# Optimization experiments

Measured on AMD Instinct MI355X. Metric: run time of the kernel, lower is better.

The kernel has to match this reference:

```python
import math
import jax, jax.numpy as jnp
import numpy as np

B, N, G, D = 8, 1000, 1000, 2
E, H = 128, 8           # embedding_dim, n_heads
DH = E // H             # head dim
KNN = 16                # n_decoding_neighbors (static: mask all zeros -> K=min(16,N))
TANH_CLIP = 10.0


def make_heads(x, n_heads):
    # (B, n, E) -> (B, n_heads, n, E//n_heads)
    b, n, e = x.shape
    return x.reshape(b, n, n_heads, e // n_heads).transpose(0, 2, 1, 3)


def setup_inputs() -> dict:
    key = jax.random.key(0)
    ks = jax.random.split(key, 12)
    s = 1.0 / math.sqrt(E)
    return {
        "last_node": jax.random.randint(ks[0], (B, G), 0, N),
        "coordinates": jax.random.uniform(ks[1], (B, N, D), dtype=jnp.float32),
        "embeddings": jax.random.normal(ks[2], (B, N, E), dtype=jnp.float32),
        "group_ninf_mask": jnp.zeros((B, G, N), dtype=jnp.float32),
        "Wq_graph": jax.random.normal(ks[3], (E, E), dtype=jnp.float32) * s,
        "Wq_first": jax.random.normal(ks[4], (E, E), dtype=jnp.float32) * s,
        "Wq_last": jax.random.normal(ks[5], (E, E), dtype=jnp.float32) * s,
        "Wk": jax.random.normal(ks[6], (E, E), dtype=jnp.float32) * s,
        "Wv": jax.random.normal(ks[7], (E, E), dtype=jnp.float32) * s,
        "W_comb": jax.random.normal(ks[8], (E, E), dtype=jnp.float32) * s,
        "b_comb": jax.random.normal(ks[9], (E,), dtype=jnp.float32) * s,
    }


def reference(last_node, coordinates, embeddings, group_ninf_mask,
              Wq_graph, Wq_first, Wq_last, Wk, Wv, W_comb, b_comb):
    # --- reset() precomputation ---
    graph_emb = embeddings.mean(axis=1, keepdims=True)          # (B,1,E)
    q_graph = make_heads(graph_emb @ Wq_graph.T, H)             # (B,H,1,DH)
    k_h = make_heads(embeddings @ Wk.T, H)                      # (B,H,N,DH)
    v_h = make_heads(embeddings @ Wv.T, H)                      # (B,H,N,DH)

    # --- gather last node embedding ---
    idx_e = jnp.broadcast_to(last_node[..., None], (B, G, E))
    last_emb = jnp.take_along_axis(embeddings, idx_e, axis=1)   # (B,G,E)
    q_first = make_heads(last_emb @ Wq_first.T, H)              # (B,H,G,DH)
    q_last = make_heads(last_emb @ Wq_last.T, H)
    glimpse_q = q_graph + q_first + q_last                      # (B,H,G,DH)

    # --- KNN neighbor mask (cdist + topk + scatter) ---
    idx_c = jnp.broadcast_to(last_node[..., None], (B, G, D))
    last_coord = jnp.take_along_axis(coordinates, idx_c, axis=1)  # (B,G,D)
    d2 = (jnp.sum(last_coord**2, -1)[:, :, None]
          + jnp.sum(coordinates**2, -1)[:, None, :]
          - 2.0 * jnp.einsum('bgd,bnd->bgn', last_coord, coordinates))
    dist = jnp.sqrt(jnp.maximum(d2, 0.0))                       # (B,G,N)
    dist = jnp.where(group_ninf_mask == -jnp.inf, jnp.inf, dist)
    _, knn_idx = jax.lax.top_k(-dist, KNN)                      # (B,G,K) smallest dists
    bi = jnp.arange(B)[:, None, None]
    gi = jnp.arange(G)[None, :, None]
    glimpse_mask = jnp.full((B, G, N), -jnp.inf, dtype=jnp.float32)
    glimpse_mask = glimpse_mask.at[bi, gi, knn_idx].set(0.0)

    # --- masked multi-head glimpse attention ---
    scores = jnp.einsum('bhgd,bhnd->bhgn', glimpse_q, k_h) / math.sqrt(DH)
    scores = scores + glimpse_mask[:, None, :, :]
    attn = jax.nn.softmax(scores, axis=-1)
    out = jnp.einsum('bhgn,bhnd->bhgd', attn, v_h)              # (B,H,G,DH)
    out = out.transpose(0, 2, 1, 3).reshape(B, G, E)
    final_q = out @ W_comb.T + b_comb                           # (B,G,E)

    # --- tanh-clipped scoring + softmax ---
    score = jnp.einsum('bge,bne->bgn', final_q, embeddings) / math.sqrt(E)
    score_masked = TANH_CLIP * jnp.tanh(score) + group_ninf_mask
    probs = jax.nn.softmax(score_masked, axis=2)                # (B,G,N)
    return probs
```

## Files before the change

kernel.cpp:

```cpp
#include <hip/hip_runtime.h>
#include <math.h>

#define BD 8
#define NN 1000
#define GG 1000
#define EE 128

typedef unsigned long long u64;

#define OFF_QG    0
#define OFF_K     1024
#define OFF_V     (OFF_K + 1024000)
#define OFF_QFL   (OFF_V + 1024000)
#define OFF_OUTG  (OFF_QFL + 1024000)
#define OFF_FQ    (OFF_OUTG + 1024000)
#define OFF_PART  (OFF_FQ + 1024000)
#define OFF_GPART (OFF_PART + 64000)

__global__ __launch_bounds__(256) void k_gq1(const float* __restrict__ emb,
                                             float* __restrict__ gpart) {
  __shared__ float ps[2][128];
  int b = blockIdx.x, blk = blockIdx.y;
  int t = threadIdx.x;
  int e = t & 127, p = t >> 7;
  const float* eb = emb + ((size_t)b * NN + blk * 40 + p * 20) * EE + e;
  float s = 0.f;
#pragma unroll 4
  for (int n = 0; n < 20; ++n) s += eb[(size_t)n * EE];
  ps[p][e] = s;
  __syncthreads();
  if (t < 128) gpart[(b * 25 + blk) * 128 + t] = ps[0][t] + ps[1][t];
}

__global__ __launch_bounds__(128) void k_gq2(const float* __restrict__ gpart,
                                             const float* __restrict__ Wqg,
                                             float* __restrict__ qg) {
  __shared__ float ge[128];
  int b = blockIdx.x, t = threadIdx.x;
  float s = 0.f;
#pragma unroll 5
  for (int j = 0; j < 25; ++j) s += gpart[(b * 25 + j) * 128 + t];
  ge[t] = s * (1.f / 1000.f);
  __syncthreads();
  const float* wr = Wqg + (size_t)t * EE;
  float acc = 0.f;
#pragma unroll 8
  for (int k = 0; k < 128; ++k) acc += ge[k] * wr[k];
  qg[b * EE + t] = acc;
}

__global__ __launch_bounds__(256) void k_proj(const float* __restrict__ emb,
                                              const float* __restrict__ Wk,
                                              const float* __restrict__ Wv,
                                              const float* __restrict__ Wqf,
                                              const float* __restrict__ Wql,
                                              float* __restrict__ Karr,
                                              float* __restrict__ Varr,
                                              float* __restrict__ QFL) {
  __shared__ float Als[16][68];
  __shared__ float Bls[16][68];
  int mt = blockIdx.x, nt = blockIdx.y;
  int t = threadIdx.x;
  int ty = t >> 4, tx = t & 15;
  int row4 = t >> 2, kq = t & 3;
  float acc[4][4] = {};
  for (int k0 = 0; k0 < 128; k0 += 16) {
    const float* ap = emb + (size_t)(mt * 64 + row4) * EE + k0 + kq * 4;
    float4 av = *(const float4*)ap;
    int j = nt * 64 + row4;
    float4 bv;
    if (j < 128) {
      bv = *(const float4*)(Wk + (size_t)j * EE + k0 + kq * 4);
    } else if (j < 256) {
      bv = *(const float4*)(Wv + (size_t)(j - 128) * EE + k0 + kq * 4);
    } else {
      float4 f = *(const float4*)(Wqf + (size_t)(j - 256) * EE + k0 + kq * 4);
      float4 l = *(const float4*)(Wql + (size_t)(j - 256) * EE + k0 + kq * 4);
      bv = make_float4(f.x + l.x, f.y + l.y, f.z + l.z, f.w + l.w);
    }
    Als[kq * 4 + 0][row4] = av.x; Als[kq * 4 + 1][row4] = av.y;
    Als[kq * 4 + 2][row4] = av.z; Als[kq * 4 + 3][row4] = av.w;
    Bls[kq * 4 + 0][row4] = bv.x; Bls[kq * 4 + 1][row4] = bv.y;
    Bls[kq * 4 + 2][row4] = bv.z; Bls[kq * 4 + 3][row4] = bv.w;
    __syncthreads();
#pragma unroll
    for (int k = 0; k < 16; ++k) {
      float a0 = Als[k][ty * 4 + 0], a1 = Als[k][ty * 4 + 1];
      float a2 = Als[k][ty * 4 + 2], a3 = Als[k][ty * 4 + 3];
      float b0 = Bls[k][tx * 4 + 0], b1 = Bls[k][tx * 4 + 1];
      float b2 = Bls[k][tx * 4 + 2], b3 = Bls[k][tx * 4 + 3];
      acc[0][0] += a0 * b0; acc[0][1] += a0 * b1; acc[0][2] += a0 * b2; acc[0][3] += a0 * b3;
      acc[1][0] += a1 * b0; acc[1][1] += a1 * b1; acc[1][2] += a1 * b2; acc[1][3] += a1 * b3;
      acc[2][0] += a2 * b0; acc[2][1] += a2 * b1; acc[2][2] += a2 * b2; acc[2][3] += a2 * b3;
      acc[3][0] += a3 * b0; acc[3][1] += a3 * b1; acc[3][2] += a3 * b2; acc[3][3] += a3 * b3;
    }
    __syncthreads();
  }
  float* outp; int cb;
  if (nt < 2)      { outp = Karr; cb = nt * 64; }
  else if (nt < 4) { outp = Varr; cb = (nt - 2) * 64; }
  else             { outp = QFL;  cb = (nt - 4) * 64; }
#pragma unroll
  for (int i = 0; i < 4; ++i) {
    int r = mt * 64 + ty * 4 + i;
    float4 v = make_float4(acc[i][0], acc[i][1], acc[i][2], acc[i][3]);
    *(float4*)(outp + (size_t)r * EE + cb + tx * 4) = v;
  }
}

template <int CTRL>
__device__ __forceinline__ unsigned dpp_minu(unsigned x) {
  unsigned o = (unsigned)__builtin_amdgcn_update_dpp(0, (int)x, CTRL, 0xf, 0xf, false);
  return o < x ? o : x;
}
__device__ __forceinline__ unsigned wave_min_u32(unsigned x) {
  x = dpp_minu<0x121>(x);
  x = dpp_minu<0x122>(x);
  x = dpp_minu<0x124>(x);
  x = dpp_minu<0x128>(x);
  unsigned o = (unsigned)__shfl_xor((int)x, 16); x = o < x ? o : x;
  o = (unsigned)__shfl_xor((int)x, 32); x = o < x ? o : x;
  return x;
}

__global__ __launch_bounds__(256) void k_glimpse(const int* __restrict__ last_node,
                                                 const float* __restrict__ coords,
                                                 const float* __restrict__ mask,
                                                 const float* __restrict__ qg,
                                                 const float* __restrict__ QFL,
                                                 const float* __restrict__ Karr,
                                                 const float* __restrict__ Varr,
                                                 float* __restrict__ outg) {
  __shared__ float pbuf[4][128];
  __shared__ int   nbuf[4][16];
  const float INF = __builtin_inff();
  int wv = threadIdx.x >> 6;
  int lane = threadIdx.x & 63;
  int wid = (blockIdx.x * blockDim.x + threadIdx.x) >> 6;
  int b = wid / GG, g = wid % GG;
  int last = last_node[b * GG + g];
  const float2* cb2 = (const float2*)(coords + (size_t)b * NN * 2);
  float2 lc = cb2[last];
  float lc2 = lc.x * lc.x + lc.y * lc.y;
  const float* mrow = mask + ((size_t)b * GG + g) * NN;
  unsigned d2u[16];
#pragma unroll
  for (int i = 0; i < 16; ++i) {
    int n = lane + (i << 6);
    unsigned k = 0xFFFFFFFFu;
    if (n < NN) {
      float2 c = cb2[n];
      float d2 = lc2 + (c.x * c.x + c.y * c.y) - 2.f * (lc.x * c.x + lc.y * c.y);
      d2 = fmaxf(d2, 0.f);
      k = __float_as_uint(d2);
      if (mrow[n] == -INF) k = 0x7F800000u;
    }
    d2u[i] = k;
  }
  int h = lane >> 3;
  int kk = lane & 7;
  int n0sel = 0, n1sel = 0;
  for (int s = 0; s < 16; ++s) {
    unsigned bv = d2u[0]; int bs = 0;
#pragma unroll
    for (int i = 1; i < 16; ++i) {
      bool better = d2u[i] < bv;
      bv = better ? d2u[i] : bv;
      bs = better ? i : bs;
    }
    unsigned wm = wave_min_u32(bv);
    u64 tied = __ballot(bv == wm);
    int wn;
    if (__popcll(tied) == 1) {
      int wl = (int)__builtin_ctzll(tied);
      int ws = __builtin_amdgcn_readlane(bs, wl);
      wn = wl + (ws << 6);
    } else {
      unsigned cn = (bv == wm) ? (unsigned)(lane + (bs << 6)) : 0x7FFFFFFFu;
      cn = wave_min_u32(cn);
      wn = (int)__builtin_amdgcn_readfirstlane((int)cn);
    }
    n0sel = (s == kk) ? wn : n0sel;
    n1sel = (s == kk + 8) ? wn : n1sel;
    int iw = wn >> 6;
    bool me = (lane == (wn & 63));
#pragma unroll
    for (int i = 0; i < 16; ++i)
      if (i == iw && me) d2u[i] = 0xFFFFFFFFu;
  }
  float qh[16];
  {
    const float4* qg4 = (const float4*)(qg + b * EE + h * 16);
    const float4* qf4 = (const float4*)(QFL + ((size_t)b * NN + last) * EE + h * 16);
#pragma unroll
    for (int u = 0; u < 4; ++u) {
      float4 a = qg4[u], c = qf4[u];
      qh[u * 4 + 0] = a.x + c.x; qh[u * 4 + 1] = a.y + c.y;
      qh[u * 4 + 2] = a.z + c.z; qh[u * 4 + 3] = a.w + c.w;
    }
  }
  const float* Kb = Karr + (size_t)b * NN * EE;
  float s0 = 0.f, s1 = 0.f;
  {
    const float4* k04 = (const float4*)(Kb + (size_t)n0sel * EE + h * 16);
    const float4* k14 = (const float4*)(Kb + (size_t)n1sel * EE + h * 16);
    float4 ka[4], kb[4];
#pragma unroll
    for (int u = 0; u < 4; ++u) { ka[u] = k04[u]; kb[u] = k14[u]; }
#pragma unroll
    for (int u = 0; u < 4; ++u) {
      s0 += qh[u * 4 + 0] * ka[u].x; s0 += qh[u * 4 + 1] * ka[u].y;
      s0 += qh[u * 4 + 2] * ka[u].z; s0 += qh[u * 4 + 3] * ka[u].w;
      s1 += qh[u * 4 + 0] * kb[u].x; s1 += qh[u * 4 + 1] * kb[u].y;
      s1 += qh[u * 4 + 2] * kb[u].z; s1 += qh[u * 4 + 3] * kb[u].w;
    }
  }
  s0 *= 0.25f; s1 *= 0.25f;
  float m = fmaxf(s0, s1);
#pragma unroll
  for (int off = 1; off < 8; off <<= 1) m = fmaxf(m, __shfl_xor(m, off));
  float e0 = __expf(s0 - m), e1 = __expf(s1 - m);
  float se = e0 + e1;
#pragma unroll
  for (int off = 1; off < 8; off <<= 1) se += __shfl_xor(se, off);
  float p0 = e0 / se, p1 = e1 / se;
  pbuf[wv][h * 16 + kk] = p0;
  pbuf[wv][h * 16 + kk + 8] = p1;
  if (h == 0) { nbuf[wv][kk] = n0sel; nbuf[wv][kk + 8] = n1sel; }
  const float* Vb = Varr + (size_t)b * NN * EE;
  float o0 = 0.f, o1 = 0.f;
#pragma unroll
  for (int c = 0; c < 2; ++c) {
    int nk[8]; float pk[8]; float2 vv[8];
#pragma unroll
    for (int j = 0; j < 8; ++j) { nk[j] = nbuf[wv][c * 8 + j]; pk[j] = pbuf[wv][h * 16 + c * 8 + j]; }
#pragma unroll
    for (int j = 0; j < 8; ++j)
      vv[j] = *(const float2*)(Vb + (size_t)nk[j] * EE + h * 16 + kk * 2);
#pragma unroll
    for (int j = 0; j < 8; ++j) { o0 += pk[j] * vv[j].x; o1 += pk[j] * vv[j].y; }
  }
  *(float2*)(outg + ((size_t)b * GG + g) * EE + h * 16 + kk * 2) = make_float2(o0, o1);
}

__global__ __launch_bounds__(256) void k_comb(const float* __restrict__ outg,
                                              const float* __restrict__ Wc,
                                              const float* __restrict__ bc,
                                              float* __restrict__ fq) {
  __shared__ float Als[16][68];
  __shared__ float Bls[16][68];
  int mt = blockIdx.x, nt = blockIdx.y;
  int t = threadIdx.x;
  int ty = t >> 4, tx = t & 15;
  int row4 = t >> 2, kq = t & 3;
  float acc[4][4] = {};
  for (int k0 = 0; k0 < 128; k0 += 16) {
    float4 av = *(const float4*)(outg + (size_t)(mt * 64 + row4) * EE + k0 + kq * 4);
    int j = nt * 64 + row4;
    float4 bv = *(const float4*)(Wc + (size_t)j * EE + k0 + kq * 4);
    Als[kq * 4 + 0][row4] = av.x; Als[kq * 4 + 1][row4] = av.y;
    Als[kq * 4 + 2][row4] = av.z; Als[kq * 4 + 3][row4] = av.w;
    Bls[kq * 4 + 0][row4] = bv.x; Bls[kq * 4 + 1][row4] = bv.y;
    Bls[kq * 4 + 2][row4] = bv.z; Bls[kq * 4 + 3][row4] = bv.w;
    __syncthreads();
#pragma unroll
    for (int k = 0; k < 16; ++k) {
      float a0 = Als[k][ty * 4 + 0], a1 = Als[k][ty * 4 + 1];
      float a2 = Als[k][ty * 4 + 2], a3 = Als[k][ty * 4 + 3];
      float b0 = Bls[k][tx * 4 + 0], b1 = Bls[k][tx * 4 + 1];
      float b2 = Bls[k][tx * 4 + 2], b3 = Bls[k][tx * 4 + 3];
      acc[0][0] += a0 * b0; acc[0][1] += a0 * b1; acc[0][2] += a0 * b2; acc[0][3] += a0 * b3;
      acc[1][0] += a1 * b0; acc[1][1] += a1 * b1; acc[1][2] += a1 * b2; acc[1][3] += a1 * b3;
      acc[2][0] += a2 * b0; acc[2][1] += a2 * b1; acc[2][2] += a2 * b2; acc[2][3] += a2 * b3;
      acc[3][0] += a3 * b0; acc[3][1] += a3 * b1; acc[3][2] += a3 * b2; acc[3][3] += a3 * b3;
    }
    __syncthreads();
  }
#pragma unroll
  for (int i = 0; i < 4; ++i) {
    int r = mt * 64 + ty * 4 + i;
    int c = nt * 64 + tx * 4;
    float4 v = make_float4(acc[i][0] + bc[c + 0], acc[i][1] + bc[c + 1],
                           acc[i][2] + bc[c + 2], acc[i][3] + bc[c + 3]);
    *(float4*)(fq + (size_t)r * EE + c) = v;
  }
}

__global__ __launch_bounds__(256, 4) void k_score(const float* __restrict__ fq,
                                                  const float* __restrict__ emb,
                                                  const float* __restrict__ mask,
                                                  float* __restrict__ out,
                                                  float* __restrict__ part) {
  __shared__ float As[16][68];
  __shared__ float Bs[16][132];
  int nt = blockIdx.x, gt = blockIdx.y, b = blockIdx.z;
  int t = threadIdx.x;
  int tx = t & 15, ty = t >> 4;
  int g0 = gt * 64, n0 = nt * 128;
  const float* A = fq + (size_t)b * GG * EE;
  const float* Bm = emb + (size_t)b * NN * EE;
  int la = t >> 2, akq = t & 3;
  int lb = t >> 1, bkq = t & 1;
  int ar = min(g0 + la, GG - 1);
  int br = min(n0 + lb, NN - 1);
  const float* apos = A + (size_t)ar * EE + akq * 4;
  const float* bpos = Bm + (size_t)br * EE + bkq * 8;

  float acc[4][8] = {};
  float4 pa  = *(const float4*)apos;
  float4 pb0 = *(const float4*)bpos;
  float4 pb1 = *(const float4*)(bpos + 4);
  for (int k0 = 0; k0 < 128; k0 += 16) {
    __syncthreads();
    As[akq * 4 + 0][la] = pa.x;  As[akq * 4 + 1][la] = pa.y;
    As[akq * 4 + 2][la] = pa.z;  As[akq * 4 + 3][la] = pa.w;
    Bs[bkq * 8 + 0][lb] = pb0.x; Bs[bkq * 8 + 1][lb] = pb0.y;
    Bs[bkq * 8 + 2][lb] = pb0.z; Bs[bkq * 8 + 3][lb] = pb0.w;
    Bs[bkq * 8 + 4][lb] = pb1.x; Bs[bkq * 8 + 5][lb] = pb1.y;
    Bs[bkq * 8 + 6][lb] = pb1.z; Bs[bkq * 8 + 7][lb] = pb1.w;
    __syncthreads();
    if (k0 < 112) {
      pa  = *(const float4*)(apos + k0 + 16);
      pb0 = *(const float4*)(bpos + k0 + 16);
      pb1 = *(const float4*)(bpos + k0 + 20);
    }
#pragma unroll
    for (int k = 0; k < 16; ++k) {
      float4 av  = *(const float4*)&As[k][ty * 4];
      float4 bv0 = *(const float4*)&Bs[k][tx * 4];
      float4 bv1 = *(const float4*)&Bs[k][64 + tx * 4];
      float af[4] = {av.x, av.y, av.z, av.w};
      float bf[8] = {bv0.x, bv0.y, bv0.z, bv0.w, bv1.x, bv1.y, bv1.z, bv1.w};
#pragma unroll
      for (int i = 0; i < 4; ++i)
#pragma unroll
        for (int j = 0; j < 8; ++j) acc[i][j] += af[i] * bf[j];
    }
  }

  const float rs = 0.08838834764831845f;
  const float NEGINF = -__builtin_inff();
  int gbase = g0 + ty * 4;
  int nb0 = n0 + tx * 4;
  int nb1 = n0 + 64 + tx * 4;
  bool b1full = (nb1 + 3 < NN);
#pragma unroll
  for (int i = 0; i < 4; ++i) {
    int g = gbase + i;
    bool gv = (g < GG);
    int gc = gv ? g : GG - 1;
    const float* mrow = mask + ((size_t)b * GG + gc) * NN;
    float* orow = out + ((size_t)b * GG + gc) * NN;
    float rsum = 0.f;
    {
      float4 m0 = *(const float4*)(mrow + nb0);
      float mv[4] = {m0.x, m0.y, m0.z, m0.w};
      float e[4];
#pragma unroll
      for (int j = 0; j < 4; ++j) {
        float sc = acc[i][j] * rs;
        float u = __expf(2.f * sc);
        float th = 1.f - 2.f * __builtin_amdgcn_rcpf(u + 1.f);
        e[j] = __expf(10.f * th + mv[j]);
        rsum += e[j];
      }
      if (gv) *(float4*)(orow + nb0) = make_float4(e[0], e[1], e[2], e[3]);
    }
    {
      float mv[4];
      if (b1full) {
        float4 m1 = *(const float4*)(mrow + nb1);
        mv[0] = m1.x; mv[1] = m1.y; mv[2] = m1.z; mv[3] = m1.w;
      } else {
#pragma unroll
        for (int j = 0; j < 4; ++j) mv[j] = (nb1 + j < NN) ? mrow[nb1 + j] : NEGINF;
      }
      float e[4];
#pragma unroll
      for (int j = 0; j < 4; ++j) {
        float sc = acc[i][4 + j] * rs;
        float u = __expf(2.f * sc);
        float th = 1.f - 2.f * __builtin_amdgcn_rcpf(u + 1.f);
        e[j] = __expf(10.f * th + mv[j]);
        rsum += e[j];
      }
      if (gv) {
        if (b1full) {
          *(float4*)(orow + nb1) = make_float4(e[0], e[1], e[2], e[3]);
        } else {
#pragma unroll
          for (int j = 0; j < 4; ++j)
            if (nb1 + j < NN) orow[nb1 + j] = e[j];
        }
      }
    }
#pragma unroll
    for (int off = 1; off < 16; off <<= 1) rsum += __shfl_xor(rsum, off);
    if (tx == 0 && gv) part[((size_t)b * GG + g) * 8 + nt] = rsum;
  }
}

__global__ __launch_bounds__(256) void k_norm(const float* __restrict__ part,
                                              float* __restrict__ out) {
  int row = blockIdx.x;
  __shared__ float ssum;
  int t = threadIdx.x;
  float v = (t < 8) ? part[(size_t)row * 8 + t] : 0.f;
#pragma unroll
  for (int off = 1; off < 8; off <<= 1) v += __shfl_xor(v, off);
  if (t == 0) ssum = v;
  __syncthreads();
  float inv = 1.f / ssum;
  if (t < 250) {
    float4* o = (float4*)(out + (size_t)row * NN);
    float4 x = o[t];
    x.x *= inv; x.y *= inv; x.z *= inv; x.w *= inv;
    o[t] = x;
  }
}

extern "C" void kernel_launch(void* const* d_in, const int* in_sizes, int n_in,
                              void* d_out, int out_size, void* d_ws, size_t ws_size,
                              hipStream_t stream) {
  const int*   last_node = (const int*)d_in[0];
  const float* coords    = (const float*)d_in[1];
  const float* emb       = (const float*)d_in[2];
  const float* mask      = (const float*)d_in[3];
  const float* Wqg       = (const float*)d_in[4];
  const float* Wqf       = (const float*)d_in[5];
  const float* Wql       = (const float*)d_in[6];
  const float* Wk        = (const float*)d_in[7];
  const float* Wv        = (const float*)d_in[8];
  const float* Wc        = (const float*)d_in[9];
  const float* bc        = (const float*)d_in[10];
  float* out = (float*)d_out;
  float* ws  = (float*)d_ws;

  float* qg    = ws + OFF_QG;
  float* Karr  = ws + OFF_K;
  float* Varr  = ws + OFF_V;
  float* QFL   = ws + OFF_QFL;
  float* outg  = ws + OFF_OUTG;
  float* fq    = ws + OFF_FQ;
  float* part  = ws + OFF_PART;
  float* gpart = ws + OFF_GPART;

  k_gq1<<<dim3(BD, 25), dim3(256), 0, stream>>>(emb, gpart);
  k_gq2<<<dim3(BD), dim3(128), 0, stream>>>(gpart, Wqg, qg);
  k_proj<<<dim3(125, 6), dim3(256), 0, stream>>>(emb, Wk, Wv, Wqf, Wql, Karr, Varr, QFL);
  k_glimpse<<<dim3(2000), dim3(256), 0, stream>>>(last_node, coords, mask, qg, QFL, Karr, Varr, outg);
  k_comb<<<dim3(125, 2), dim3(256), 0, stream>>>(outg, Wc, bc, fq);
  k_score<<<dim3(8, 16, 8), dim3(256), 0, stream>>>(fq, emb, mask, out, part);
  k_norm<<<dim3(8000), dim3(256), 0, stream>>>(part, out);
}
```

Measured before the change: 208.4 us.

## Use split-bf16 MFMA for score GEMM with pre-swizzled operand layout

Replaces the FP32 shared-memory SIMT GEMM in the score kernel with bf16 MFMA instructions. Each operand is split into three bf16 parts (high, mid, low), and six cross products keep close to FP32 accuracy. A new conversion kernel writes emb and final_q into an MFMA-fragment-ordered layout in workspace, reusing the K and QFL buffers, so the GEMM loads fragments directly without LDS. The cost is two extra launches and extra memory traffic. The epilogue now uses scalar mask loads and output stores, which are less coalesced than the previous float4 accesses.

```diff
diff --git a/kernel.cpp b/kernel.cpp
--- a/kernel.cpp
+++ b/kernel.cpp
@@ -7,6 +7,8 @@
 #define EE 128
 
 typedef unsigned long long u64;
+typedef __attribute__((ext_vector_type(8))) short short8;
+typedef __attribute__((ext_vector_type(4))) float f32x4;
 
 #define OFF_QG    0
 #define OFF_K     1024
@@ -286,117 +288,97 @@
   }
 }
 
-__global__ __launch_bounds__(256, 4) void k_score(const float* __restrict__ fq,
-                                                  const float* __restrict__ emb,
-                                                  const float* __restrict__ mask,
-                                                  float* __restrict__ out,
-                                                  float* __restrict__ part) {
-  __shared__ float As[16][68];
-  __shared__ float Bs[16][132];
+__global__ __launch_bounds__(256) void k_cvt(const float* __restrict__ src,
+                                             short* __restrict__ dst) {
+  int t = blockIdx.x, b = blockIdx.y;
+  int w = threadIdx.x >> 6, l = threadIdx.x & 63;
+  int r = min(t * 16 + (l & 15), NN - 1);
+  int k = w * 32 + (l >> 4) * 8;
+  const float* sp = src + ((size_t)b * NN + r) * EE + k;
+  float4 v0 = *(const float4*)sp;
+  float4 v1 = *(const float4*)(sp + 4);
+  float x[8] = {v0.x, v0.y, v0.z, v0.w, v1.x, v1.y, v1.z, v1.w};
+  short8 hv, mv, lv;
+#pragma unroll
+  for (int j = 0; j < 8; ++j) {
+    float xv = x[j];
+    unsigned uh = __float_as_uint(xv) & 0xFFFF0000u;
+    hv[j] = (short)(uh >> 16);
+    float r1 = xv - __uint_as_float(uh);
+    unsigned um = __float_as_uint(r1) & 0xFFFF0000u;
+    mv[j] = (short)(um >> 16);
+    float r2 = r1 - __uint_as_float(um);
+    lv[j] = (short)(__float_as_uint(r2) >> 16);
+  }
+  short* dbase = dst + ((size_t)b * 393216 + (size_t)((t * 4 + w) * 3) * 512 + l * 8);
+  *(short8*)(dbase)        = hv;
+  *(short8*)(dbase + 512)  = mv;
+  *(short8*)(dbase + 1024) = lv;
+}
+
+__global__ __launch_bounds__(256) void k_score(const short* __restrict__ fq3,
+                                               const short* __restrict__ emb3,
+                                               const float* __restrict__ mask,
+                                               float* __restrict__ out,
+                                               float* __restrict__ part) {
   int nt = blockIdx.x, gt = blockIdx.y, b = blockIdx.z;
-  int t = threadIdx.x;
-  int tx = t & 15, ty = t >> 4;
-  int g0 = gt * 64, n0 = nt * 128;
-  const float* A = fq + (size_t)b * GG * EE;
-  const float* Bm = emb + (size_t)b * NN * EE;
-  int la = t >> 2, akq = t & 3;
-  int lb = t >> 1, bkq = t & 1;
-  int ar = min(g0 + la, GG - 1);
-  int br = min(n0 + lb, NN - 1);
-  const float* apos = A + (size_t)ar * EE + akq * 4;
-  const float* bpos = Bm + (size_t)br * EE + bkq * 8;
-
-  float acc[4][8] = {};
-  float4 pa  = *(const float4*)apos;
-  float4 pb0 = *(const float4*)bpos;
-  float4 pb1 = *(const float4*)(bpos + 4);
-  for (int k0 = 0; k0 < 128; k0 += 16) {
-    __syncthreads();
-    As[akq * 4 + 0][la] = pa.x;  As[akq * 4 + 1][la] = pa.y;
-    As[akq * 4 + 2][la] = pa.z;  As[akq * 4 + 3][la] = pa.w;
-    Bs[bkq * 8 + 0][lb] = pb0.x; Bs[bkq * 8 + 1][lb] = pb0.y;
-    Bs[bkq * 8 + 2][lb] = pb0.z; Bs[bkq * 8 + 3][lb] = pb0.w;
-    Bs[bkq * 8 + 4][lb] = pb1.x; Bs[bkq * 8 + 5][lb] = pb1.y;
-    Bs[bkq * 8 + 6][lb] = pb1.z; Bs[bkq * 8 + 7][lb] = pb1.w;
-    __syncthreads();
-    if (k0 < 112) {
-      pa  = *(const float4*)(apos + k0 + 16);
-      pb0 = *(const float4*)(bpos + k0 + 16);
-      pb1 = *(const float4*)(bpos + k0 + 20);
-    }
-#pragma unroll
-    for (int k = 0; k < 16; ++k) {
-      float4 av  = *(const float4*)&As[k][ty * 4];
-      float4 bv0 = *(const float4*)&Bs[k][tx * 4];
-      float4 bv1 = *(const float4*)&Bs[k][64 + tx * 4];
-      float af[4] = {av.x, av.y, av.z, av.w};
-      float bf[8] = {bv0.x, bv0.y, bv0.z, bv0.w, bv1.x, bv1.y, bv1.z, bv1.w};
-#pragma unroll
-      for (int i = 0; i < 4; ++i)
-#pragma unroll
-        for (int j = 0; j < 8; ++j) acc[i][j] += af[i] * bf[j];
-    }
-  }
-
+  int w = threadIdx.x >> 6, l = threadIdx.x & 63;
+  int gtile = gt * 4 + w;
+  const short* ab = fq3 + ((size_t)b * 393216 + (size_t)gtile * 4 * 3 * 512 + l * 8);
+  const short* bb = emb3 + ((size_t)b * 393216 + (size_t)nt * 8 * 4 * 3 * 512 + l * 8);
+  f32x4 acc[8] = {};
+#pragma unroll
+  for (int k0 = 0; k0 < 4; ++k0) {
+    short8 ah = *(const short8*)(ab + (k0 * 3 + 0) * 512);
+    short8 am = *(const short8*)(ab + (k0 * 3 + 1) * 512);
+    short8 al = *(const short8*)(ab + (k0 * 3 + 2) * 512);
+#pragma unroll
+    for (int c = 0; c < 8; ++c) {
+      const short* bp = bb + (size_t)((c * 4 + k0) * 3) * 512;
+      short8 bh = *(const short8*)(bp);
+      short8 bm = *(const short8*)(bp + 512);
+      short8 bl = *(const short8*)(bp + 1024);
+      acc[c] = __builtin_amdgcn_mfma_f32_16x16x32_bf16(ah, bh, acc[c], 0, 0, 0);
+      acc[c] = __builtin_amdgcn_mfma_f32_16x16x32_bf16(am, bh, acc[c], 0, 0, 0);
+      acc[c] = __builtin_amdgcn_mfma_f32_16x16x32_bf16(ah, bm, acc[c], 0, 0, 0);
+      acc[c] = __builtin_amdgcn_mfma_f32_16x16x32_bf16(am, bm, acc[c], 0, 0, 0);
+      acc[c] = __builtin_amdgcn_mfma_f32_16x16x32_bf16(al, bh, acc[c], 0, 0, 0);
+      acc[c] = __builtin_amdgcn_mfma_f32_16x16x32_bf16(ah, bl, acc[c], 0, 0, 0);
+    }
+  }
   const float rs = 0.08838834764831845f;
   const float NEGINF = -__builtin_inff();
-  int gbase = g0 + ty * 4;
-  int nb0 = n0 + tx * 4;
-  int nb1 = n0 + 64 + tx * 4;
-  bool b1full = (nb1 + 3 < NN);
-#pragma unroll
-  for (int i = 0; i < 4; ++i) {
-    int g = gbase + i;
+  int q = l >> 4, cl = l & 15;
+  int gb = gt * 64 + w * 16 + q * 4;
+  size_t brow = (size_t)b * GG;
+#pragma unroll
+  for (int r = 0; r < 4; ++r) {
+    int g = gb + r;
     bool gv = (g < GG);
-    int gc = gv ? g : GG - 1;
-    const float* mrow = mask + ((size_t)b * GG + gc) * NN;
-    float* orow = out + ((size_t)b * GG + gc) * NN;
+    size_t row = (brow + (gv ? g : GG - 1)) * (size_t)NN;
     float rsum = 0.f;
-    {
-      float4 m0 = *(const float4*)(mrow + nb0);
-      float mv[4] = {m0.x, m0.y, m0.z, m0.w};
-      float e[4];
-#pragma unroll
-      for (int j = 0; j < 4; ++j) {
-        float sc = acc[i][j] * rs;
-        float u = __expf(2.f * sc);
-        float th = 1.f - 2.f * __builtin_amdgcn_rcpf(u + 1.f);
-        e[j] = __expf(10.f * th + mv[j]);
-        rsum += e[j];
+    float ev[8];
+#pragma unroll
+    for (int c = 0; c < 8; ++c) {
+      int n = nt * 128 + c * 16 + cl;
+      float mvv = (gv && n < NN) ? mask[row + n] : NEGINF;
+      float sc = acc[c][r] * rs;
+      float u = __expf(2.f * sc);
+      float th = 1.f - 2.f * __builtin_amdgcn_rcpf(u + 1.f);
+      float e = __expf(10.f * th + mvv);
+      ev[c] = e;
+      rsum += e;
+    }
+    if (gv) {
+#pragma unroll
+      for (int c = 0; c < 8; ++c) {
+        int n = nt * 128 + c * 16 + cl;
+        if (n < NN) out[row + n] = ev[c];
       }
-      if (gv) *(float4*)(orow + nb0) = make_float4(e[0], e[1], e[2], e[3]);
-    }
-    {
-      float mv[4];
-      if (b1full) {
-        float4 m1 = *(const float4*)(mrow + nb1);
-        mv[0] = m1.x; mv[1] = m1.y; mv[2] = m1.z; mv[3] = m1.w;
-      } else {
-#pragma unroll
-        for (int j = 0; j < 4; ++j) mv[j] = (nb1 + j < NN) ? mrow[nb1 + j] : NEGINF;
-      }
-      float e[4];
-#pragma unroll
-      for (int j = 0; j < 4; ++j) {
-        float sc = acc[i][4 + j] * rs;
-        float u = __expf(2.f * sc);
-        float th = 1.f - 2.f * __builtin_amdgcn_rcpf(u + 1.f);
-        e[j] = __expf(10.f * th + mv[j]);
-        rsum += e[j];
-      }
-      if (gv) {
-        if (b1full) {
-          *(float4*)(orow + nb1) = make_float4(e[0], e[1], e[2], e[3]);
-        } else {
-#pragma unroll
-          for (int j = 0; j < 4; ++j)
-            if (nb1 + j < NN) orow[nb1 + j] = e[j];
-        }
-      }
     }
 #pragma unroll
     for (int off = 1; off < 16; off <<= 1) rsum += __shfl_xor(rsum, off);
-    if (tx == 0 && gv) part[((size_t)b * GG + g) * 8 + nt] = rsum;
+    if (cl == 0 && gv) part[(brow + g) * 8 + nt] = rsum;
   }
 }
 
@@ -444,12 +426,16 @@
   float* fq    = ws + OFF_FQ;
   float* part  = ws + OFF_PART;
   float* gpart = ws + OFF_GPART;
+  short* emb3  = (short*)(ws + OFF_K);
+  short* fq3   = (short*)(ws + OFF_QFL);
 
   k_gq1<<<dim3(BD, 25), dim3(256), 0, stream>>>(emb, gpart);
   k_gq2<<<dim3(BD), dim3(128), 0, stream>>>(gpart, Wqg, qg);
   k_proj<<<dim3(125, 6), dim3(256), 0, stream>>>(emb, Wk, Wv, Wqf, Wql, Karr, Varr, QFL);
   k_glimpse<<<dim3(2000), dim3(256), 0, stream>>>(last_node, coords, mask, qg, QFL, Karr, Varr, outg);
   k_comb<<<dim3(125, 2), dim3(256), 0, stream>>>(outg, Wc, bc, fq);
-  k_score<<<dim3(8, 16, 8), dim3(256), 0, stream>>>(fq, emb, mask, out, part);
+  k_cvt<<<dim3(64, BD), dim3(256), 0, stream>>>(emb, emb3);
+  k_cvt<<<dim3(64, BD), dim3(256), 0, stream>>>(fq, fq3);
+  k_score<<<dim3(8, 16, 8), dim3(256), 0, stream>>>(fq3, emb3, mask, out, part);
   k_norm<<<dim3(8000), dim3(256), 0, stream>>>(part, out);
 }
```

Result: no change. 210.3 us (+0.9%).
